# Kernel tuning notes

Hardware: AMD Instinct MI355X
Metric: run time of the kernel (lower is better)

## Reference

```python
import jax, jax.numpy as jnp
import numpy as np


def setup_inputs() -> dict:
    B, Lq, Lk, D, F, H = 2, 2048, 2048, 128, 128, 8
    key = jax.random.key(0)
    ks = jax.random.split(key, 8)
    X_Q = jax.random.normal(ks[0], (B, Lq, D), dtype=jnp.float32)
    X_K = jax.random.normal(ks[1], (B, Lk, D), dtype=jnp.float32)
    X_V = jax.random.normal(ks[2], (B, Lk, F), dtype=jnp.float32)
    mask = jax.random.randint(ks[3], (B, 1, Lq, Lk), 0, 2, dtype=jnp.int32)
    # xavier_normal for [H, D, D]: std = sqrt(2/(D+D))
    W_Q = jax.random.normal(ks[4], (H, D, D), dtype=jnp.float32) * np.sqrt(2.0 / (D + D))
    W_K = jax.random.normal(ks[5], (H, D, D), dtype=jnp.float32) * np.sqrt(2.0 / (D + D))
    W_V = jax.random.normal(ks[6], (H, F, F), dtype=jnp.float32) * np.sqrt(2.0 / (F + F))
    O = jax.random.normal(ks[7], (F * H, F), dtype=jnp.float32) * np.sqrt(2.0 / (F * H + F))
    return {"X_Q": X_Q, "X_K": X_K, "X_V": X_V, "mask": mask,
            "W_Q": W_Q, "W_K": W_K, "W_V": W_V, "O": O}


def reference(X_Q, X_K, X_V, mask, W_Q, W_K, W_V, O):
    B, Lq, D = X_Q.shape
    H = W_Q.shape[0]
    F = W_V.shape[1]
    # torch.einsum with repeated in-operand index ('hdd') takes the diagonal
    dq = jnp.diagonal(W_Q, axis1=1, axis2=2)  # [H, D]
    dk = jnp.diagonal(W_K, axis1=1, axis2=2)  # [H, D]
    dv = jnp.diagonal(W_V, axis1=1, axis2=2)  # [H, F]
    g = dq * dk                               # fused per-head QK diagonal scale [H, D]
    scale = 1.0 / jnp.sqrt(jnp.asarray(D, dtype=X_Q.dtype))
    scores = jnp.einsum('bqd,hd,bkd->bhqk', X_Q, g, X_K) * scale  # [B,H,Lq,Lk]
    scores = jnp.where(mask == 0, jnp.asarray(-jnp.inf, scores.dtype), scores)
    A = jax.nn.softmax(scores, axis=-1)
    # O_h = A @ (diag(dv_h) scaled V)
    Oh = jnp.einsum('bhqk,hf,bkf->bhqf', A, dv, X_V)  # [B,H,Lq,F]
    Oh = Oh.transpose(0, 2, 1, 3).reshape(B, Lq, H * F)
    return jnp.einsum('bqx,xf->bqf', Oh, O)
```

## Files before the change

### kernel.cpp

```cpp
#include <hip/hip_runtime.h>

typedef __bf16 bf16;
typedef __bf16 bf16x4 __attribute__((ext_vector_type(4)));
typedef __bf16 bf16x8 __attribute__((ext_vector_type(8)));
typedef float f32x4 __attribute__((ext_vector_type(4)));
typedef short s16x4 __attribute__((ext_vector_type(4)));
typedef unsigned int u32;
typedef unsigned long long u64;

#define B_ 2
#define H_ 8
#define L_ 2048
#define D_ 128
#define F_ 128
#define QT 64
#define KT 64
#define NKT (L_ / KT)

#define WS_KB 0u
#define WS_VT (1u << 20)
#define WS_MB (2u << 20)

#define SMEM_BYTES 66048
#define LWS_OFF 65536
#define POX_STRIDE 132
#define SOH_OFF 36864
#define SOH_STRIDE 136
#define SO2_STRIDE 136

__device__ __forceinline__ void dma16(const void* g, void* l) {
    __builtin_amdgcn_global_load_lds(
        (const __attribute__((address_space(1))) u32*)g,
        (__attribute__((address_space(3))) u32*)l, 16, 0, 0);
}

__device__ __forceinline__ f32x4 mfma32(bf16x8 a, bf16x8 b, f32x4 c) {
    return __builtin_amdgcn_mfma_f32_16x16x32_bf16(a, b, c, 0, 0, 0);
}

__device__ __forceinline__ f32x4 mfma16(bf16x4 a, bf16x4 b, f32x4 c) {
#if __has_builtin(__builtin_amdgcn_mfma_f32_16x16x16_bf16)
    return __builtin_amdgcn_mfma_f32_16x16x16_bf16(a, b, c, 0, 0, 0);
#else
    s16x4 as = __builtin_bit_cast(s16x4, a);
    s16x4 bs = __builtin_bit_cast(s16x4, b);
    return __builtin_amdgcn_mfma_f32_16x16x16bf16_1k(as, bs, c, 0, 0, 0);
#endif
}

__device__ __forceinline__ float fast_exp2(float x) {
#if __has_builtin(__builtin_amdgcn_exp2f)
    return __builtin_amdgcn_exp2f(x);
#else
    return exp2f(x);
#endif
}

__global__ __launch_bounds__(256)
void prep_all(const float* __restrict__ XK, const float* __restrict__ XV,
              const int* __restrict__ mask, bf16* __restrict__ Kb,
              bf16* __restrict__ Vtb, u64* __restrict__ bits)
{
    const int bid = blockIdx.x;
    const int tid = threadIdx.x;
    if (bid < 8192) {
        int wv = bid * 4 + (tid >> 6);
        int lane = tid & 63;
        size_t base = (size_t)wv * 256;
        #pragma unroll
        for (int s = 0; s < 4; ++s) {
            int m = mask[base + s * 64 + lane];
            u64 bal = __ballot(m != 0);
            if (lane == 0) bits[(size_t)wv * 4 + s] = bal;
        }
    } else if (bid < 8448) {
        int gid = (bid - 8192) * 256 + tid;
        int row = gid >> 4;
        int j   = gid & 15;
        const float* src = XK + (size_t)row * 128 + j * 8;
        float4 v0 = *(const float4*)src;
        float4 v1 = *(const float4*)(src + 4);
        bf16x8 w;
        w[0] = (bf16)v0.x; w[1] = (bf16)v0.y; w[2] = (bf16)v0.z; w[3] = (bf16)v0.w;
        w[4] = (bf16)v1.x; w[5] = (bf16)v1.y; w[6] = (bf16)v1.z; w[7] = (bf16)v1.w;
        int jp = j ^ (row & 15);
        *(bf16x8*)(Kb + (size_t)row * 128 + jp * 8) = w;
    } else {
        int idx  = bid - 8448;
        int tile = idx >> 2;
        int fq   = idx & 3;
        int f    = fq * 32 + (tid & 31);
        int j    = tid >> 5;
        int bb   = tile >> 5, kt = tile & 31;
        const float* src = XV + ((size_t)(bb * L_ + kt * 64 + j * 8)) * F_ + f;
        bf16x4 w0, w1;
        #pragma unroll
        for (int jj = 0; jj < 4; ++jj) {
            w0[jj] = (bf16)src[(size_t)jj * F_];
            w1[jj] = (bf16)src[(size_t)(4 + jj) * F_];
        }
        bf16* outp = Vtb + (size_t)tile * 8192 + f * 64;
        *(bf16x4*)(outp + (((2 * j) ^ (f & 15)) * 4)) = w0;
        *(bf16x4*)(outp + (((2 * j + 1) ^ (f & 15)) * 4)) = w1;
    }
}

__global__ __launch_bounds__(512, 4)
void attn_fused_kernel(const float* __restrict__ XQ, const bf16* __restrict__ Kb,
                       const bf16* __restrict__ Vtb, const u64* __restrict__ bits,
                       const float* __restrict__ WQ, const float* __restrict__ WK,
                       const float* __restrict__ WV, const float* __restrict__ Om,
                       float* __restrict__ out)
{
    __shared__ __align__(16) char smem[SMEM_BYTES];
    __shared__ __align__(16) float g_s[128];

    bf16* sK0 = (bf16*)smem;
    bf16* sK1 = (bf16*)(smem + 16384);
    bf16* sV0 = (bf16*)(smem + 32768);
    bf16* sV1 = (bf16*)(smem + 49152);
    float* lws = (float*)(smem + LWS_OFF);
    float* pOx = (float*)smem;
    bf16* sOh  = (bf16*)(smem + SOH_OFF);
    bf16* sO2t = (bf16*)smem;

    const int tid  = threadIdx.x;
    const int wave = tid >> 6;
    const int lane = tid & 63;
    const int c    = lane & 15;
    const int quad = lane >> 4;
    const int qt = blockIdx.x, h = blockIdx.y, b = blockIdx.z;
    const int q0 = qt * QT;

    const int kh   = wave >> 2;
    const int msel = wave & 3;
    const int fv  = tid & 127;
    const int grp = tid >> 7;

    if (tid < 128) {
        float wq = WQ[(h * D_ + tid) * D_ + tid];
        float wk = WK[(h * D_ + tid) * D_ + tid];
        g_s[tid] = wq * wk * 0.12752230502179406f;
    }
    __syncthreads();

    const char* gK = (const char*)Kb + (size_t)(b * L_) * 256;
    const char* gV = (const char*)Vtb + (size_t)(b * NKT) * 16384;

    dma16(gK + tid * 16, (char*)sK0 + tid * 16);
    dma16(gK + 8192 + tid * 16, (char*)sK0 + 8192 + tid * 16);
    dma16(gV + tid * 16, (char*)sV0 + tid * 16);
    dma16(gV + 8192 + tid * 16, (char*)sV0 + 8192 + tid * 16);

    const u64* mrow = bits + (size_t)(b * L_ + q0 + msel * 16 + c) * NKT;
    u64 mb_cur = mrow[0];

    bf16x8 qfrag[4];
    {
        const float* qrow = XQ + (size_t)(b * L_ + q0 + msel * 16 + c) * D_;
        #pragma unroll
        for (int kc = 0; kc < 4; ++kc) {
            int d0 = kc * 32 + quad * 8;
            float4 v0 = *(const float4*)(qrow + d0);
            float4 v1 = *(const float4*)(qrow + d0 + 4);
            float4 g0 = *(const float4*)(g_s + d0);
            float4 g1 = *(const float4*)(g_s + d0 + 4);
            bf16x8 w;
            w[0] = (bf16)(v0.x * g0.x); w[1] = (bf16)(v0.y * g0.y);
            w[2] = (bf16)(v0.z * g0.z); w[3] = (bf16)(v0.w * g0.w);
            w[4] = (bf16)(v1.x * g1.x); w[5] = (bf16)(v1.y * g1.y);
            w[6] = (bf16)(v1.z * g1.z); w[7] = (bf16)(v1.w * g1.w);
            qfrag[kc] = w;
        }
    }

    f32x4 oacc[8];
    #pragma unroll
    for (int fi = 0; fi < 8; ++fi)
        #pragma unroll
        for (int r = 0; r < 4; ++r) oacc[fi][r] = 0.f;
    float lsum = 0.f;

    #pragma unroll 2
    for (int kt = 0; kt < NKT; ++kt) {
        bf16* sK  = (kt & 1) ? sK1 : sK0;
        bf16* sV  = (kt & 1) ? sV1 : sV0;
        bf16* sKn = (kt & 1) ? sK0 : sK1;
        bf16* sVn = (kt & 1) ? sV0 : sV1;

        asm volatile("s_waitcnt vmcnt(0)" ::: "memory");
        asm volatile("s_barrier" ::: "memory");

        if (kt + 1 < NKT) {
            const char* gkn = gK + (size_t)(kt + 1) * 16384;
            const char* gvn = gV + (size_t)(kt + 1) * 16384;
            dma16(gkn + tid * 16, (char*)sKn + tid * 16);
            dma16(gkn + 8192 + tid * 16, (char*)sKn + 8192 + tid * 16);
            dma16(gvn + tid * 16, (char*)sVn + tid * 16);
            dma16(gvn + 8192 + tid * 16, (char*)sVn + 8192 + tid * 16);
        }
        u64 mb_next = mrow[(kt + 1 < NKT) ? kt + 1 : kt];

        f32x4 tacc[2];
        #pragma unroll
        for (int kti = 0; kti < 2; ++kti)
            #pragma unroll
            for (int r = 0; r < 4; ++r) tacc[kti][r] = 0.f;

        #pragma unroll
        for (int kti = 0; kti < 2; ++kti) {
            const bf16* krow = sK + ((kh * 2 + kti) * 16 + c) * 128;
            #pragma unroll
            for (int kc = 0; kc < 4; ++kc) {
                bf16x8 kfrag = *(const bf16x8*)(krow + (((kc * 4 + quad) ^ c) * 8));
                tacc[kti] = mfma32(kfrag, qfrag[kc], tacc[kti]);
            }
        }

        bf16x4 pfrag[2];
        #pragma unroll
        for (int kti = 0; kti < 2; ++kti) {
            #pragma unroll
            for (int r = 0; r < 4; ++r) {
                int pos = kh * 32 + kti * 16 + quad * 4 + r;
                float p = ((mb_cur >> pos) & 1ull) ? fast_exp2(tacc[kti][r]) : 0.f;
                lsum += p;
                pfrag[kti][r] = (bf16)p;
            }
        }

        #pragma unroll
        for (int fi = 0; fi < 8; ++fi) {
            #pragma unroll
            for (int kti = 0; kti < 2; ++kti) {
                int g = kh * 8 + kti * 4 + quad;
                bf16x4 vfrag = *(const bf16x4*)(sV + (fi * 16 + c) * 64 + ((g ^ c) * 4));
                oacc[fi] = mfma16(pfrag[kti], vfrag, oacc[fi]);
            }
        }

        mb_cur = mb_next;
    }

    {
        float v = lsum;
        v += __shfl_xor(v, 16); v += __shfl_xor(v, 32);
        if (lane < 16) lws[wave * 16 + lane] = v;
    }
    if (tid < 128)
        g_s[tid] = WV[(h * F_ + tid) * F_ + tid];
    __syncthreads();

    if (kh == 1) {
        #pragma unroll
        for (int fi = 0; fi < 8; ++fi)
            #pragma unroll
            for (int r = 0; r < 4; ++r)
                pOx[(msel * 16 + quad * 4 + r) * POX_STRIDE + fi * 16 + c] = oacc[fi][r];
    }
    __syncthreads();

    if (kh == 0) {
        float linv[4];
        #pragma unroll
        for (int r = 0; r < 4; ++r) {
            int m16 = quad * 4 + r;
            linv[r] = 1.0f / (lws[msel * 16 + m16] + lws[(4 + msel) * 16 + m16]);
        }
        #pragma unroll
        for (int fi = 0; fi < 8; ++fi)
            #pragma unroll
            for (int r = 0; r < 4; ++r) {
                int row = msel * 16 + quad * 4 + r;
                float v = (oacc[fi][r] + pOx[row * POX_STRIDE + fi * 16 + c]) * linv[r];
                sOh[row * SOH_STRIDE + fi * 16 + c] = (bf16)v;
            }
    }
    __syncthreads();

    #pragma unroll
    for (int i = 0; i < 8; ++i) {
        int fp4 = grp * 32 + i * 4;
        bf16x4 w;
        #pragma unroll
        for (int j = 0; j < 4; ++j) {
            int x = fp4 + j;
            w[j] = (bf16)(Om[(h * F_ + x) * F_ + fv] * g_s[x]);
        }
        *(bf16x4*)(sO2t + fv * SO2_STRIDE + fp4) = w;
    }
    __syncthreads();

    const int pm = wave & 3;
    const int pf = wave >> 2;
    bf16x8 afr[4];
    const bf16* ohrow = sOh + (pm * 16 + c) * SOH_STRIDE;
    #pragma unroll
    for (int kc = 0; kc < 4; ++kc)
        afr[kc] = *(const bf16x8*)(ohrow + kc * 32 + quad * 8);

    #pragma unroll
    for (int nt = 0; nt < 4; ++nt) {
        f32x4 pacc;
        #pragma unroll
        for (int r = 0; r < 4; ++r) pacc[r] = 0.f;
        const bf16* orow = sO2t + ((pf * 4 + nt) * 16 + c) * SO2_STRIDE;
        #pragma unroll
        for (int kc = 0; kc < 4; ++kc) {
            bf16x8 bfrag = *(const bf16x8*)(orow + kc * 32 + quad * 8);
            pacc = mfma32(afr[kc], bfrag, pacc);
        }
        #pragma unroll
        for (int r = 0; r < 4; ++r) {
            int qg = q0 + pm * 16 + quad * 4 + r;
            atomicAdd(out + ((size_t)(b * L_ + qg) * F_ + (pf * 4 + nt) * 16 + c), pacc[r]);
        }
    }
}

extern "C" void kernel_launch(void* const* d_in, const int* in_sizes, int n_in,
                              void* d_out, int out_size, void* d_ws, size_t ws_size,
                              hipStream_t stream) {
    const float* XQ   = (const float*)d_in[0];
    const float* XK   = (const float*)d_in[1];
    const float* XV   = (const float*)d_in[2];
    const int*   mask = (const int*)d_in[3];
    const float* WQ   = (const float*)d_in[4];
    const float* WK   = (const float*)d_in[5];
    const float* WV   = (const float*)d_in[6];
    const float* Om   = (const float*)d_in[7];
    float* out = (float*)d_out;

    char* ws = (char*)d_ws;
    bf16* Kb   = (bf16*)(ws + WS_KB);
    bf16* Vtb  = (bf16*)(ws + WS_VT);
    u64*  bits = (u64*)(ws + WS_MB);

    prep_all<<<8704, 256, 0, stream>>>(XK, XV, mask, Kb, Vtb, bits);
    hipMemsetAsync(out, 0, (size_t)out_size * sizeof(float), stream);

    dim3 grid(L_ / QT, H_, B_);
    attn_fused_kernel<<<grid, 512, 0, stream>>>(XQ, Kb, Vtb, bits, WQ, WK, WV, Om, out);
}
```

Measured before the change: 165.5 us.

## Split key tile four ways across waves with two query subtiles per wave

Reorganises the attention work split so each wave handles 16 keys and 32 query rows, with two M subtiles sharing each K and V fragment load. The aim is to halve LDS fragment reads per MFMA. The cost is twice the accumulator registers and a longer multi-stage cross-wave reduction through shared memory. It also folds output zeroing into the prep kernel in place of a memset, and relaxes the DMA wait to vmcnt(6) before a second barrier so the mask loads can be issued early. Risks are register pressure at the 4-blocks launch bound and the correctness of the new waitcnt counts.

```diff
diff --git a/kernel.cpp b/kernel.cpp
--- a/kernel.cpp
+++ b/kernel.cpp
@@ -6,6 +6,7 @@
 typedef float f32x4 __attribute__((ext_vector_type(4)));
 typedef short s16x4 __attribute__((ext_vector_type(4)));
 typedef unsigned int u32;
+typedef unsigned short u16;
 typedef unsigned long long u64;
 
 #define B_ 2
@@ -21,12 +22,15 @@
 #define WS_VT (1u << 20)
 #define WS_MB (2u << 20)
 
-#define SMEM_BYTES 66048
-#define LWS_OFF 65536
-#define POX_STRIDE 132
-#define SOH_OFF 36864
+#define SMEM_BYTES 67584
+#define POXA_OFF 0
+#define POXB_OFF 33280
+#define POX_STRIDE 130
+#define SOH_OFF 0
 #define SOH_STRIDE 136
+#define SO2_OFF 17408
 #define SO2_STRIDE 136
+#define LWS_OFF 66560
 
 __device__ __forceinline__ void dma16(const void* g, void* l) {
     __builtin_amdgcn_global_load_lds(
@@ -59,7 +63,8 @@
 __global__ __launch_bounds__(256)
 void prep_all(const float* __restrict__ XK, const float* __restrict__ XV,
               const int* __restrict__ mask, bf16* __restrict__ Kb,
-              bf16* __restrict__ Vtb, u64* __restrict__ bits)
+              bf16* __restrict__ Vtb, u64* __restrict__ bits,
+              float* __restrict__ outz)
 {
     const int bid = blockIdx.x;
     const int tid = threadIdx.x;
@@ -85,7 +90,7 @@
         w[4] = (bf16)v1.x; w[5] = (bf16)v1.y; w[6] = (bf16)v1.z; w[7] = (bf16)v1.w;
         int jp = j ^ (row & 15);
         *(bf16x8*)(Kb + (size_t)row * 128 + jp * 8) = w;
-    } else {
+    } else if (bid < 8704) {
         int idx  = bid - 8448;
         int tile = idx >> 2;
         int fq   = idx & 3;
@@ -102,6 +107,12 @@
         bf16* outp = Vtb + (size_t)tile * 8192 + f * 64;
         *(bf16x4*)(outp + (((2 * j) ^ (f & 15)) * 4)) = w0;
         *(bf16x4*)(outp + (((2 * j + 1) ^ (f & 15)) * 4)) = w1;
+    } else {
+        int idx = bid - 8704;
+        float4* o4 = (float4*)outz + (size_t)idx * 2048 + tid;
+        float4 z = {0.f, 0.f, 0.f, 0.f};
+        #pragma unroll
+        for (int i = 0; i < 8; ++i) o4[i * 256] = z;
     }
 }
 
@@ -119,10 +130,11 @@
     bf16* sK1 = (bf16*)(smem + 16384);
     bf16* sV0 = (bf16*)(smem + 32768);
     bf16* sV1 = (bf16*)(smem + 49152);
+    float* pOxA = (float*)(smem + POXA_OFF);
+    float* pOxB = (float*)(smem + POXB_OFF);
+    bf16* sOh  = (bf16*)(smem + SOH_OFF);
+    bf16* sO2t = (bf16*)(smem + SO2_OFF);
     float* lws = (float*)(smem + LWS_OFF);
-    float* pOx = (float*)smem;
-    bf16* sOh  = (bf16*)(smem + SOH_OFF);
-    bf16* sO2t = (bf16*)smem;
 
     const int tid  = threadIdx.x;
     const int wave = tid >> 6;
@@ -132,8 +144,8 @@
     const int qt = blockIdx.x, h = blockIdx.y, b = blockIdx.z;
     const int q0 = qt * QT;
 
-    const int kh   = wave >> 2;
-    const int msel = wave & 3;
+    const int kh   = wave >> 1;
+    const int msel = wave & 1;
     const int fv  = tid & 127;
     const int grp = tid >> 7;
 
@@ -152,12 +164,13 @@
     dma16(gV + tid * 16, (char*)sV0 + tid * 16);
     dma16(gV + 8192 + tid * 16, (char*)sV0 + 8192 + tid * 16);
 
-    const u64* mrow = bits + (size_t)(b * L_ + q0 + msel * 16 + c) * NKT;
-    u64 mb_cur = mrow[0];
-
-    bf16x8 qfrag[4];
-    {
-        const float* qrow = XQ + (size_t)(b * L_ + q0 + msel * 16 + c) * D_;
+    const u16* mrow0 = (const u16*)(bits + (size_t)(b * L_ + q0 + msel * 32 + c) * NKT) + kh;
+    const u16* mrow1 = mrow0 + (size_t)16 * NKT * 4;
+
+    bf16x8 qfrag[2][4];
+    #pragma unroll
+    for (int mi = 0; mi < 2; ++mi) {
+        const float* qrow = XQ + (size_t)(b * L_ + q0 + msel * 32 + mi * 16 + c) * D_;
         #pragma unroll
         for (int kc = 0; kc < 4; ++kc) {
             int d0 = kc * 32 + quad * 8;
@@ -170,16 +183,18 @@
             w[2] = (bf16)(v0.z * g0.z); w[3] = (bf16)(v0.w * g0.w);
             w[4] = (bf16)(v1.x * g1.x); w[5] = (bf16)(v1.y * g1.y);
             w[6] = (bf16)(v1.z * g1.z); w[7] = (bf16)(v1.w * g1.w);
-            qfrag[kc] = w;
-        }
-    }
-
-    f32x4 oacc[8];
-    #pragma unroll
-    for (int fi = 0; fi < 8; ++fi)
-        #pragma unroll
-        for (int r = 0; r < 4; ++r) oacc[fi][r] = 0.f;
-    float lsum = 0.f;
+            qfrag[mi][kc] = w;
+        }
+    }
+
+    f32x4 oacc[2][8];
+    #pragma unroll
+    for (int mi = 0; mi < 2; ++mi)
+        #pragma unroll
+        for (int fi = 0; fi < 8; ++fi)
+            #pragma unroll
+            for (int r = 0; r < 4; ++r) oacc[mi][fi][r] = 0.f;
+    float lsum[2] = {0.f, 0.f};
 
     #pragma unroll 2
     for (int kt = 0; kt < NKT; ++kt) {
@@ -188,8 +203,10 @@
         bf16* sKn = (kt & 1) ? sK0 : sK1;
         bf16* sVn = (kt & 1) ? sV0 : sV1;
 
-        asm volatile("s_waitcnt vmcnt(0)" ::: "memory");
         asm volatile("s_barrier" ::: "memory");
+
+        u32 mh0 = mrow0[(size_t)kt * 4];
+        u32 mh1 = mrow1[(size_t)kt * 4];
 
         if (kt + 1 < NKT) {
             const char* gkn = gK + (size_t)(kt + 1) * 16384;
@@ -198,83 +215,121 @@
             dma16(gkn + 8192 + tid * 16, (char*)sKn + 8192 + tid * 16);
             dma16(gvn + tid * 16, (char*)sVn + tid * 16);
             dma16(gvn + 8192 + tid * 16, (char*)sVn + 8192 + tid * 16);
-        }
-        u64 mb_next = mrow[(kt + 1 < NKT) ? kt + 1 : kt];
+            asm volatile("s_waitcnt vmcnt(6)" ::: "memory");
+        } else {
+            asm volatile("s_waitcnt vmcnt(2)" ::: "memory");
+        }
+        asm volatile("s_barrier" ::: "memory");
 
         f32x4 tacc[2];
         #pragma unroll
-        for (int kti = 0; kti < 2; ++kti)
-            #pragma unroll
-            for (int r = 0; r < 4; ++r) tacc[kti][r] = 0.f;
-
-        #pragma unroll
-        for (int kti = 0; kti < 2; ++kti) {
-            const bf16* krow = sK + ((kh * 2 + kti) * 16 + c) * 128;
-            #pragma unroll
-            for (int kc = 0; kc < 4; ++kc) {
-                bf16x8 kfrag = *(const bf16x8*)(krow + (((kc * 4 + quad) ^ c) * 8));
-                tacc[kti] = mfma32(kfrag, qfrag[kc], tacc[kti]);
+        for (int mi = 0; mi < 2; ++mi)
+            #pragma unroll
+            for (int r = 0; r < 4; ++r) tacc[mi][r] = 0.f;
+
+        const bf16* krow = sK + (kh * 16 + c) * 128;
+        #pragma unroll
+        for (int kc = 0; kc < 4; ++kc) {
+            bf16x8 kfrag = *(const bf16x8*)(krow + (((kc * 4 + quad) ^ c) * 8));
+            tacc[0] = mfma32(kfrag, qfrag[0][kc], tacc[0]);
+            tacc[1] = mfma32(kfrag, qfrag[1][kc], tacc[1]);
+        }
+
+        bf16x4 pfrag[2];
+        #pragma unroll
+        for (int mi = 0; mi < 2; ++mi) {
+            u32 mh = mi ? mh1 : mh0;
+            #pragma unroll
+            for (int r = 0; r < 4; ++r) {
+                int pos = quad * 4 + r;
+                float p = ((mh >> pos) & 1u) ? fast_exp2(tacc[mi][r]) : 0.f;
+                lsum[mi] += p;
+                pfrag[mi][r] = (bf16)p;
             }
         }
 
-        bf16x4 pfrag[2];
-        #pragma unroll
-        for (int kti = 0; kti < 2; ++kti) {
-            #pragma unroll
-            for (int r = 0; r < 4; ++r) {
-                int pos = kh * 32 + kti * 16 + quad * 4 + r;
-                float p = ((mb_cur >> pos) & 1ull) ? fast_exp2(tacc[kti][r]) : 0.f;
-                lsum += p;
-                pfrag[kti][r] = (bf16)p;
-            }
-        }
-
         #pragma unroll
         for (int fi = 0; fi < 8; ++fi) {
-            #pragma unroll
-            for (int kti = 0; kti < 2; ++kti) {
-                int g = kh * 8 + kti * 4 + quad;
-                bf16x4 vfrag = *(const bf16x4*)(sV + (fi * 16 + c) * 64 + ((g ^ c) * 4));
-                oacc[fi] = mfma16(pfrag[kti], vfrag, oacc[fi]);
-            }
-        }
-
-        mb_cur = mb_next;
-    }
-
-    {
-        float v = lsum;
+            int g = kh * 4 + quad;
+            bf16x4 vfrag = *(const bf16x4*)(sV + (fi * 16 + c) * 64 + ((g ^ c) * 4));
+            oacc[0][fi] = mfma16(pfrag[0], vfrag, oacc[0][fi]);
+            oacc[1][fi] = mfma16(pfrag[1], vfrag, oacc[1][fi]);
+        }
+    }
+
+    #pragma unroll
+    for (int mi = 0; mi < 2; ++mi) {
+        float v = lsum[mi];
         v += __shfl_xor(v, 16); v += __shfl_xor(v, 32);
-        if (lane < 16) lws[wave * 16 + lane] = v;
+        if (lane < 16) lws[wave * 32 + mi * 16 + lane] = v;
     }
     if (tid < 128)
         g_s[tid] = WV[(h * F_ + tid) * F_ + tid];
     __syncthreads();
 
-    if (kh == 1) {
-        #pragma unroll
-        for (int fi = 0; fi < 8; ++fi)
-            #pragma unroll
-            for (int r = 0; r < 4; ++r)
-                pOx[(msel * 16 + quad * 4 + r) * POX_STRIDE + fi * 16 + c] = oacc[fi][r];
+    if (kh == 2) {
+        #pragma unroll
+        for (int mi = 0; mi < 2; ++mi)
+            #pragma unroll
+            for (int fi = 0; fi < 8; ++fi)
+                #pragma unroll
+                for (int r = 0; r < 4; ++r)
+                    pOxA[(msel * 32 + mi * 16 + quad * 4 + r) * POX_STRIDE + fi * 16 + c]
+                        = oacc[mi][fi][r];
+    } else if (kh == 3) {
+        #pragma unroll
+        for (int mi = 0; mi < 2; ++mi)
+            #pragma unroll
+            for (int fi = 0; fi < 8; ++fi)
+                #pragma unroll
+                for (int r = 0; r < 4; ++r)
+                    pOxB[(msel * 32 + mi * 16 + quad * 4 + r) * POX_STRIDE + fi * 16 + c]
+                        = oacc[mi][fi][r];
     }
     __syncthreads();
 
     if (kh == 0) {
-        float linv[4];
-        #pragma unroll
-        for (int r = 0; r < 4; ++r) {
-            int m16 = quad * 4 + r;
-            linv[r] = 1.0f / (lws[msel * 16 + m16] + lws[(4 + msel) * 16 + m16]);
-        }
-        #pragma unroll
-        for (int fi = 0; fi < 8; ++fi)
+        #pragma unroll
+        for (int mi = 0; mi < 2; ++mi)
+            #pragma unroll
+            for (int fi = 0; fi < 8; ++fi)
+                #pragma unroll
+                for (int r = 0; r < 4; ++r)
+                    oacc[mi][fi][r] += pOxA[(msel * 32 + mi * 16 + quad * 4 + r) * POX_STRIDE + fi * 16 + c];
+    } else if (kh == 1) {
+        #pragma unroll
+        for (int mi = 0; mi < 2; ++mi)
+            #pragma unroll
+            for (int fi = 0; fi < 8; ++fi)
+                #pragma unroll
+                for (int r = 0; r < 4; ++r) {
+                    int a = (msel * 32 + mi * 16 + quad * 4 + r) * POX_STRIDE + fi * 16 + c;
+                    pOxB[a] += oacc[mi][fi][r];
+                }
+    }
+    __syncthreads();
+
+    if (kh == 0) {
+        #pragma unroll
+        for (int mi = 0; mi < 2; ++mi) {
+            float linv[4];
             #pragma unroll
             for (int r = 0; r < 4; ++r) {
-                int row = msel * 16 + quad * 4 + r;
-                float v = (oacc[fi][r] + pOx[row * POX_STRIDE + fi * 16 + c]) * linv[r];
-                sOh[row * SOH_STRIDE + fi * 16 + c] = (bf16)v;
+                int m16 = mi * 16 + quad * 4 + r;
+                float s = lws[msel * 32 + m16]        + lws[64 + msel * 32 + m16]
+                        + lws[128 + msel * 32 + m16]  + lws[192 + msel * 32 + m16];
+                linv[r] = 1.0f / s;
             }
+            #pragma unroll
+            for (int fi = 0; fi < 8; ++fi)
+                #pragma unroll
+                for (int r = 0; r < 4; ++r) {
+                    int row = msel * 32 + mi * 16 + quad * 4 + r;
+                    float v = (oacc[mi][fi][r]
+                               + pOxB[row * POX_STRIDE + fi * 16 + c]) * linv[r];
+                    sOh[row * SOH_STRIDE + fi * 16 + c] = (bf16)v;
+                }
+        }
     }
     __syncthreads();
 
@@ -336,8 +391,7 @@
     bf16* Vtb  = (bf16*)(ws + WS_VT);
     u64*  bits = (u64*)(ws + WS_MB);
 
-    prep_all<<<8704, 256, 0, stream>>>(XK, XV, mask, Kb, Vtb, bits);
-    hipMemsetAsync(out, 0, (size_t)out_size * sizeof(float), stream);
+    prep_all<<<8768, 256, 0, stream>>>(XK, XV, mask, Kb, Vtb, bits, out);
 
     dim3 grid(L_ / QT, H_, B_);
     attn_fused_kernel<<<grid, 512, 0, stream>>>(XQ, Kb, Vtb, bits, WQ, WK, WV, Om, out);
```

Measured after the change: 367.4 us. +122.1%, slower.
